# Kernel optimization log

Measured on AMD Instinct MI355X. Metric: run time of the kernel, lower is better.

## Reference

```python
import jax, jax.numpy as jnp
import numpy as np

B, H, W, C = 2, 64, 64, 256
G, K, L = 16, 9, 2
Cg = C // G


def _ln(x, g, b, eps=1e-6):
    m = jnp.mean(x, -1, keepdims=True)
    v = jnp.mean((x - m) ** 2, -1, keepdims=True)
    return (x - m) * jax.lax.rsqrt(v + eps) * g + b


def _conv(x, w, b=None, groups=1):
    y = jax.lax.conv_general_dilated(x, w, (1, 1), 'SAME',
        dimension_numbers=('NHWC', 'HWIO', 'NHWC'), feature_group_count=groups)
    return y if b is None else y + b


def _gelu(x):
    return jax.nn.gelu(x, approximate=False)  # torch nn.GELU (exact erf)


def _dcnv3(x, dw_w, dw_b, dwn_g, dwn_b, off_w, off_b, msk_w, msk_b,
           inp_w, inp_b, out_w, out_b, offset_scale=1.0):
    # x: [B,H,W,C] channels-last. kernel=3, stride=1, pad=1, dilation=1.
    xp = x @ inp_w + inp_b                                   # input_proj
    f = _gelu(_ln(_conv(x, dw_w, dw_b, groups=C), dwn_g, dwn_b))  # dw_conv branch
    off = (f @ off_w + off_b).reshape(B, H, W, G, K, 2) * offset_scale  # pixel units (x,y)
    mask = jax.nn.softmax((f @ msk_w + msk_b).reshape(B, H, W, G, K), axis=-1)
    dy, dx = jnp.meshgrid(jnp.arange(3.0) - 1.0, jnp.arange(3.0) - 1.0, indexing='ij')
    gx = dx.reshape(-1)
    gy = dy.reshape(-1)  # [K] kernel dilation grid
    # sampling locations in the zero-padded (pad=1) frame; pixel i center = i+0.5
    loc_x = (jnp.arange(W, dtype=x.dtype) + 1.5)[None, None, :, None, None] + gx + off[..., 0]
    loc_y = (jnp.arange(H, dtype=x.dtype) + 1.5)[None, :, None, None, None] + gy + off[..., 1]
    xg = jnp.pad(xp, ((0, 0), (1, 1), (1, 1), (0, 0))).reshape(B, H + 2, W + 2, G, Cg)
    px = loc_x - 0.5
    py = loc_y - 0.5
    x0 = jnp.floor(px).astype(jnp.int32)
    y0 = jnp.floor(py).astype(jnp.int32)
    fx = (px - x0)[..., None]
    fy = (py - y0)[..., None]
    Hp, Wp = H + 2, W + 2
    bi = jnp.arange(B).reshape(B, 1, 1, 1, 1)
    gi = jnp.arange(G).reshape(1, 1, 1, G, 1)

    def gather(yi, xi):  # zero padding outside bounds (grid_sample padding_mode='zeros')
        ok = ((yi >= 0) & (yi < Hp) & (xi >= 0) & (xi < Wp)).astype(x.dtype)[..., None]
        return xg[bi, jnp.clip(yi, 0, Hp - 1), jnp.clip(xi, 0, Wp - 1), gi] * ok

    top = gather(y0, x0) * (1 - fx) + gather(y0, x0 + 1) * fx
    bot = gather(y0 + 1, x0) * (1 - fx) + gather(y0 + 1, x0 + 1) * fx
    samp = top * (1 - fy) + bot * fy                         # [B,H,W,G,K,Cg]
    out = (samp * mask[..., None]).sum(4).reshape(B, H, W, C)
    return out @ out_w + out_b                               # output_proj


def _leffn(x, dc_w, dc_b, g, b, c1_w, c1_b, c2_w, c2_b, gamma):
    y = _ln(_conv(x, dc_w, dc_b, groups=C), g, b)
    y = _gelu(y @ c1_w + c1_b) @ c2_w + c2_b
    return x + gamma * y


def _cbam(x, w1, w2, sa_w, g, b):
    fc = lambda v: jax.nn.relu(v @ w1) @ w2
    ca = jax.nn.sigmoid(fc(x.mean((1, 2))) + fc(x.max((1, 2))))[:, None, None, :]
    x = x * ca
    sm = jnp.stack([x.mean(-1), x.max(-1)], -1)              # [B,H,W,2]
    x = x * jax.nn.sigmoid(_conv(sm, sa_w))
    return _ln(x, g, b)


def _upsample(x, w, bb, g, bt):
    y = jax.image.resize(x, (B, 2 * H, 2 * W, C), 'bilinear')  # align_corners=False
    y = _conv(y, w, bb)                                        # 3x3, C -> C//2
    return _gelu(_ln(y, g, bt))


def _forward(x, ln1_g, ln1_b, dw_w, dw_b, dwn_g, dwn_b, off_w, off_b, msk_w, msk_b,
             inp_w, inp_b, out_w, out_b, ln2_g, ln2_b, dc_w, dc_b, fn_g, fn_b,
             c1_w, c1_b, c2_w, c2_b, ffn_gamma, ca_w1, ca_w2, sa_w, cb_g, cb_b,
             nf_g, nf_b, up_w, up_b, up_g, up_bt):
    x = _cbam(x, ca_w1, ca_w2, sa_w, cb_g, cb_b)
    for i in range(L):  # fixed small depth; structural loop
        x = x + _dcnv3(_ln(x, ln1_g[i], ln1_b[i]), dw_w[i], dw_b[i], dwn_g[i], dwn_b[i],
                       off_w[i], off_b[i], msk_w[i], msk_b[i], inp_w[i], inp_b[i],
                       out_w[i], out_b[i])
        x = x + _leffn(_ln(x, ln2_g[i], ln2_b[i]), dc_w[i], dc_b[i], fn_g[i], fn_b[i],
                       c1_w[i], c1_b[i], c2_w[i], c2_b[i], ffn_gamma[i])
    x = _ln(x, nf_g, nf_b)
    return _upsample(x, up_w, up_b, up_g, up_bt)


def setup_inputs() -> dict:
    ks = iter(jax.random.split(jax.random.key(0), 80))
    r = lambda shp, s=0.02: jax.random.normal(next(ks), shp, dtype=jnp.float32) * s
    one = lambda shp: jnp.ones(shp, jnp.float32)
    zero = lambda shp: jnp.zeros(shp, jnp.float32)
    return dict(
        x=jax.random.normal(next(ks), (B, H, W, C), dtype=jnp.float32),
        ln1_g=one((L, C)), ln1_b=zero((L, C)),
        dw_w=r((L, 3, 3, 1, C)), dw_b=zero((L, C)),
        dwn_g=one((L, C)), dwn_b=zero((L, C)),
        off_w=r((L, C, G * K * 2), 0.01), off_b=zero((L, G * K * 2)),
        msk_w=r((L, C, G * K)), msk_b=zero((L, G * K)),
        inp_w=r((L, C, C)), inp_b=zero((L, C)),
        out_w=r((L, C, C)), out_b=zero((L, C)),
        ln2_g=one((L, C)), ln2_b=zero((L, C)),
        dc_w=r((L, 7, 7, 1, C)), dc_b=zero((L, C)),
        fn_g=one((L, C)), fn_b=zero((L, C)),
        c1_w=r((L, C, 4 * C)), c1_b=zero((L, 4 * C)),
        c2_w=r((L, 4 * C, C)), c2_b=zero((L, C)),
        ffn_gamma=0.7 * one((L, C)),
        ca_w1=r((C, C // 16)), ca_w2=r((C // 16, C)),
        sa_w=r((7, 7, 2, 1)),
        cb_g=one((C,)), cb_b=zero((C,)),
        nf_g=one((C,)), nf_b=zero((C,)),
        up_w=r((3, 3, C, C // 2)), up_b=zero((C // 2,)),
        up_g=one((C // 2,)), up_bt=zero((C // 2,)),
    )


def reference(x, ln1_g, ln1_b, dw_w, dw_b, dwn_g, dwn_b, off_w, off_b, msk_w, msk_b,
              inp_w, inp_b, out_w, out_b, ln2_g, ln2_b, dc_w, dc_b, fn_g, fn_b,
              c1_w, c1_b, c2_w, c2_b, ffn_gamma, ca_w1, ca_w2, sa_w, cb_g, cb_b,
              nf_g, nf_b, up_w, up_b, up_g, up_bt):
    return _forward(x, ln1_g, ln1_b, dw_w, dw_b, dwn_g, dwn_b, off_w, off_b, msk_w, msk_b,
                    inp_w, inp_b, out_w, out_b, ln2_g, ln2_b, dc_w, dc_b, fn_g, fn_b,
                    c1_w, c1_b, c2_w, c2_b, ffn_gamma, ca_w1, ca_w2, sa_w, cb_g, cb_b,
                    nf_g, nf_b, up_w, up_b, up_g, up_bt)
```

## Files before the change

### kernel.cpp

```cpp
#include <hip/hip_runtime.h>
#include <math.h>

#define B_ 2
#define H_ 64
#define W_ 64
#define C_ 256
#define G_ 16
#define HW_ (H_*W_)
#define M_ (B_*HW_)
#define C4_ (4*C_)
#define OFFN_ 288
#define MSKN_ 144
#define OMN_ 432
#define UH_ 128
#define UW_ 128
#define MUP_ (B_*UH_*UW_)
#define KUP_ (9*C_)
#define NOUT_ 128

typedef short short8 __attribute__((ext_vector_type(8)));
typedef float f32x4 __attribute__((ext_vector_type(4)));
typedef unsigned short us4 __attribute__((ext_vector_type(4)));

__device__ __forceinline__ float gelu_f(float x){
  return 0.5f * x * (1.f + erff(x * 0.70710678118654752440f));
}
__device__ __forceinline__ float sigmoid_f(float x){ return 1.f/(1.f+expf(-x)); }
__device__ __forceinline__ unsigned short f2bf(float x){
  unsigned int u = __float_as_uint(x);
  unsigned int r = (u + 0x7fffu + ((u>>16)&1u)) >> 16;
  return (unsigned short)r;
}
__device__ __forceinline__ float bf2f(unsigned short u){
  return __uint_as_float(((unsigned int)u) << 16);
}
__device__ __forceinline__ float bfl(unsigned int u){ return __uint_as_float(u<<16); }
__device__ __forceinline__ float bfh(unsigned int u){ return __uint_as_float(u & 0xffff0000u); }
__device__ __forceinline__ unsigned int pk(float a, float b){
  return (unsigned int)f2bf(a) | ((unsigned int)f2bf(b) << 16);
}

__device__ __forceinline__ void block_sum2(float& s, float& ss, float* sm){
  #pragma unroll
  for (int off=32; off>0; off>>=1){ s += __shfl_down(s, off); ss += __shfl_down(ss, off); }
  int lane = threadIdx.x & 63, wid = threadIdx.x >> 6;
  if (lane == 0){ sm[wid] = s; sm[4+wid] = ss; }
  __syncthreads();
  float a = 0.f, b = 0.f;
  int nw = blockDim.x >> 6;
  for (int i=0;i<nw;i++){ a += sm[i]; b += sm[4+i]; }
  s = a; ss = b;
}

__device__ __forceinline__ void block_summax(float& s, float& m, float* sm){
  #pragma unroll
  for (int off=32; off>0; off>>=1){ s += __shfl_down(s, off); m = fmaxf(m, __shfl_down(m, off)); }
  int lane = threadIdx.x & 63, wid = threadIdx.x >> 6;
  if (lane == 0){ sm[wid] = s; sm[4+wid] = m; }
  __syncthreads();
  float a = 0.f, b = -3.4e38f;
  int nw = blockDim.x >> 6;
  for (int i=0;i<nw;i++){ a += sm[i]; b = fmaxf(b, sm[4+i]); }
  s = a; m = b;
}

#define NJOBS 13
struct WtJobs {
  const float* src[NJOBS];
  unsigned short* dst[NJOBS];
  int Kd[NJOBS], Nd[NJOBS];
  int tOff[NJOBS+1];
};

__global__ __launch_bounds__(256) void k_wt_all(WtJobs J){
  __shared__ float tile[32][33];
  int bid = blockIdx.x;
  int j = 0;
  while (bid >= J.tOff[j+1]) j++;
  int lt = bid - J.tOff[j];
  const float* W = J.src[j];
  unsigned short* Wt = J.dst[j];
  int Kd = J.Kd[j], Nd = J.Nd[j];
  int ktiles = Kd >> 5;
  int k0 = (lt % ktiles) * 32, n0 = (lt / ktiles) * 32;
  int t = threadIdx.x;
  int r = t>>3, c4 = (t&7)*4;
  float4 v = make_float4(0.f,0.f,0.f,0.f);
  if (n0 + c4 < Nd) v = *(const float4*)(W + (size_t)(k0+r)*Nd + n0 + c4);
  tile[c4+0][r]=v.x; tile[c4+1][r]=v.y; tile[c4+2][r]=v.z; tile[c4+3][r]=v.w;
  __syncthreads();
  if (n0 + r < Nd){
    us4 o;
    o.x = f2bf(tile[r][c4+0]); o.y = f2bf(tile[r][c4+1]);
    o.z = f2bf(tile[r][c4+2]); o.w = f2bf(tile[r][c4+3]);
    *(us4*)(Wt + (size_t)(n0+r)*Kd + k0 + c4) = o;
  }
}

__global__ __launch_bounds__(256) void k_chpool(const float* __restrict__ Xin,
      float* __restrict__ psum, float* __restrict__ pmax){
  int chunk = blockIdx.x, b = blockIdx.y; int c = threadIdx.x;
  const float* p = Xin + (((size_t)b*HW_) + chunk*32)*C_ + c;
  float s = 0.f, m = -3.4e38f;
  for (int i=0;i<32;i++){ float v = p[(size_t)i*C_]; s += v; m = fmaxf(m, v); }
  psum[(b*128+chunk)*C_+c] = s; pmax[(b*128+chunk)*C_+c] = m;
}

__global__ __launch_bounds__(512) void k_ca(const float* __restrict__ psum, const float* __restrict__ pmax,
    const float* __restrict__ w1, const float* __restrict__ w2, float* __restrict__ ca){
  __shared__ float pm[2][256], px[2][256], hh[2][2][16];
  int t = threadIdx.x;
  {
    int b = t >> 8, c = t & 255;
    float s = 0.f, m = -3.4e38f;
    for (int ch=0; ch<128; ch++){ s += psum[(b*128+ch)*256+c]; m = fmaxf(m, pmax[(b*128+ch)*256+c]); }
    pm[b][c] = s * (1.f/4096.f); px[b][c] = m;
  }
  __syncthreads();
  if (t < 64){
    int b = t >> 5, typ = (t >> 4) & 1, j = t & 15;
    const float* src = typ ? px[b] : pm[b];
    float a = 0.f;
    for (int c2=0;c2<256;c2++) a += src[c2]*w1[c2*16+j];
    hh[b][typ][j] = fmaxf(a, 0.f);
  }
  __syncthreads();
  {
    int b = t >> 8, c = t & 255;
    float a = 0.f;
    for (int j=0;j<16;j++) a += (hh[b][0][j]+hh[b][1][j]) * w2[j*256+c];
    ca[b*256+c] = sigmoid_f(a);
  }
}

__global__ __launch_bounds__(256) void k_apply_ca(const float* __restrict__ Xin, float* __restrict__ X,
    const float* __restrict__ ca, float* __restrict__ smean, float* __restrict__ smax){
  __shared__ float sm[12];
  int pix = blockIdx.x, c = threadIdx.x;
  int b = pix >> 12;
  float v = Xin[(size_t)pix*C_+c] * ca[b*C_+c];
  X[(size_t)pix*C_+c] = v;
  float s = v, m = v;
  block_summax(s, m, sm);
  if (c == 0){ smean[pix] = s * (1.f/C_); smax[pix] = m; }
}

__global__ __launch_bounds__(256) void k_sa(const float* __restrict__ smean, const float* __restrict__ smax,
    const float* __restrict__ w, float* __restrict__ sa){
  int pix = blockIdx.x*256 + threadIdx.x;
  if (pix >= M_) return;
  int b = pix >> 12, hw = pix & 4095, h = hw >> 6, ww = hw & 63;
  float s = 0.f;
  for (int ky=0;ky<7;ky++){
    int hh = h + ky - 3; if (hh < 0 || hh >= H_) continue;
    for (int kx=0;kx<7;kx++){
      int xx = ww + kx - 3; if (xx < 0 || xx >= W_) continue;
      int q = (b<<12) + (hh<<6) + xx;
      s += smean[q]*w[(ky*7+kx)*2+0] + smax[q]*w[(ky*7+kx)*2+1];
    }
  }
  sa[pix] = sigmoid_f(s);
}

__global__ __launch_bounds__(256) void k_mul_ln_ln1(float* __restrict__ X, const float* __restrict__ sa,
    const float* __restrict__ g, const float* __restrict__ b,
    const float* __restrict__ g1, const float* __restrict__ b1, unsigned short* __restrict__ Tb){
  __shared__ float sm[12];
  int pix = blockIdx.x, c = threadIdx.x;
  float v = X[(size_t)pix*C_+c] * sa[pix];
  float s = v, ss = v*v;
  block_sum2(s, ss, sm);
  float mean = s * (1.f/C_), var = ss*(1.f/C_) - mean*mean;
  float r = rsqrtf(var + 1e-6f);
  float x0 = (v-mean)*r*g[c] + b[c];
  X[(size_t)pix*C_+c] = x0;
  __syncthreads();
  s = x0; ss = x0*x0;
  block_sum2(s, ss, sm);
  mean = s * (1.f/C_); var = ss*(1.f/C_) - mean*mean;
  r = rsqrtf(var + 1e-6f);
  Tb[(size_t)pix*C_+c] = f2bf((x0-mean)*r*g1[c] + b1[c]);
}

template<int KS, int DOGELU>
__global__ __launch_bounds__(256) void k_dwconv(const unsigned short* __restrict__ T,
    unsigned short* __restrict__ Out,
    const float* __restrict__ w, const float* __restrict__ bias,
    const float* __restrict__ g, const float* __restrict__ bb){
  constexpr int R = KS/2;
  int t = blockIdx.x*256 + threadIdx.x;
  int pix = t >> 5, grp = t & 31;
  int c0 = grp*8;
  int b = pix >> 12, hw = pix & 4095, h = hw >> 6, ww = hw & 63;
  float acc[8];
  {
    float4 b0 = *(const float4*)(bias + c0), b1 = *(const float4*)(bias + c0 + 4);
    acc[0]=b0.x; acc[1]=b0.y; acc[2]=b0.z; acc[3]=b0.w;
    acc[4]=b1.x; acc[5]=b1.y; acc[6]=b1.z; acc[7]=b1.w;
  }
  const unsigned short* tb = T + ((size_t)b*HW_)*C_ + c0;
  for (int ky=0;ky<KS;ky++){
    int hh = h + ky - R; if (hh < 0 || hh >= H_) continue;
    for (int kx=0;kx<KS;kx++){
      int xx = ww + kx - R; if (xx < 0 || xx >= W_) continue;
      uint4 a = *(const uint4*)(tb + ((size_t)hh*W_+xx)*C_);
      const float* wp = w + (ky*KS+kx)*C_ + c0;
      float4 w0 = *(const float4*)wp, w1 = *(const float4*)(wp+4);
      acc[0] += bfl(a.x)*w0.x; acc[1] += bfh(a.x)*w0.y;
      acc[2] += bfl(a.y)*w0.z; acc[3] += bfh(a.y)*w0.w;
      acc[4] += bfl(a.z)*w1.x; acc[5] += bfh(a.z)*w1.y;
      acc[6] += bfl(a.w)*w1.z; acc[7] += bfh(a.w)*w1.w;
    }
  }
  float s = 0.f, ss = 0.f;
  #pragma unroll
  for (int i=0;i<8;i++){ s += acc[i]; ss += acc[i]*acc[i]; }
  #pragma unroll
  for (int off=1; off<32; off<<=1){ s += __shfl_xor(s, off); ss += __shfl_xor(ss, off); }
  float mean = s * (1.f/C_), var = ss*(1.f/C_) - mean*mean;
  float r = rsqrtf(var + 1e-6f);
  float4 g0 = *(const float4*)(g + c0), g1 = *(const float4*)(g + c0 + 4);
  float4 p0 = *(const float4*)(bb + c0), p1 = *(const float4*)(bb + c0 + 4);
  float o[8];
  o[0]=(acc[0]-mean)*r*g0.x+p0.x; o[1]=(acc[1]-mean)*r*g0.y+p0.y;
  o[2]=(acc[2]-mean)*r*g0.z+p0.z; o[3]=(acc[3]-mean)*r*g0.w+p0.w;
  o[4]=(acc[4]-mean)*r*g1.x+p1.x; o[5]=(acc[5]-mean)*r*g1.y+p1.y;
  o[6]=(acc[6]-mean)*r*g1.z+p1.z; o[7]=(acc[7]-mean)*r*g1.w+p1.w;
  if (DOGELU){
    #pragma unroll
    for (int i=0;i<8;i++) o[i] = gelu_f(o[i]);
  }
  uint4 ov;
  ov.x = pk(o[0],o[1]); ov.y = pk(o[2],o[3]); ov.z = pk(o[4],o[5]); ov.w = pk(o[6],o[7]);
  *(uint4*)(Out + (size_t)pix*C_ + c0) = ov;
}

template<int TM, int EP, int OUTBF>
__global__ __launch_bounds__(256) void k_gemm_mfma(
    const unsigned short* __restrict__ A, const unsigned short* __restrict__ Bt,
    void* __restrict__ OutV, const float* __restrict__ bias,
    const float* __restrict__ bias2, int Ni, int Ki)
{
  constexpr int LD = 40;
  __shared__ unsigned short As[TM*LD];
  __shared__ unsigned short Bs[128*LD];
  const int tid = threadIdx.x;
  const int wave = tid >> 6, lane = tid & 63;
  const int m0 = blockIdx.x * TM, n0 = blockIdx.y * 128;
  const int wm0 = (wave >> 1) * (TM/2);
  const int wn0 = (wave & 1) * 64;
  constexpr int MI = TM/32;
  f32x4 acc[MI][4] = {};
  const int lm = lane & 15, kq = lane >> 4;
  constexpr int ACH = TM*4/256;

  for (int k0 = 0; k0 < Ki; k0 += 32){
    #pragma unroll
    for (int i=0;i<ACH;i++){
      int ch = tid*ACH + i;
      int r = ch >> 2, cc = (ch & 3) << 3;
      short8 v = *(const short8*)(A + (size_t)(m0 + r)*Ki + k0 + cc);
      *(short8*)(As + r*LD + cc) = v;
    }
    #pragma unroll
    for (int i=0;i<2;i++){
      int ch = tid + 256*i;
      int r = ch >> 2, cc = (ch & 3) << 3;
      short8 v = {};
      if (n0 + r < Ni) v = *(const short8*)(Bt + (size_t)(n0 + r)*Ki + k0 + cc);
      *(short8*)(Bs + r*LD + cc) = v;
    }
    __syncthreads();
    short8 af[MI], bf[4];
    #pragma unroll
    for (int mi=0;mi<MI;mi++) af[mi] = *(const short8*)(As + (wm0 + mi*16 + lm)*LD + kq*8);
    #pragma unroll
    for (int ni=0;ni<4;ni++)  bf[ni] = *(const short8*)(Bs + (wn0 + ni*16 + lm)*LD + kq*8);
    #pragma unroll
    for (int mi=0;mi<MI;mi++)
      #pragma unroll
      for (int ni=0;ni<4;ni++)
        acc[mi][ni] = __builtin_amdgcn_mfma_f32_16x16x32_bf16(af[mi], bf[ni], acc[mi][ni], 0,0,0);
    __syncthreads();
  }
  #pragma unroll
  for (int mi=0;mi<MI;mi++){
    #pragma unroll
    for (int ni=0;ni<4;ni++){
      int n = n0 + wn0 + ni*16 + lm;
      if (n < Ni){
        float bv;
        if constexpr (EP==4) bv = (n < OFFN_) ? bias[n] : bias2[n-OFFN_];
        else bv = bias[n];
        #pragma unroll
        for (int r=0;r<4;r++){
          int m = m0 + wm0 + mi*16 + kq*4 + r;
          size_t o = (size_t)m*Ni + n;
          float v = acc[mi][ni][r] + bv;
          if constexpr (EP==1) v = gelu_f(v);
          if constexpr (OUTBF) ((unsigned short*)OutV)[o] = f2bf(v);
          else                 ((float*)OutV)[o] = v;
        }
      }
    }
  }
}

template<int EP>
__global__ __launch_bounds__(256) void k_gemm_ln(
    const unsigned short* __restrict__ A, const unsigned short* __restrict__ Bt,
    float* __restrict__ X, const float* __restrict__ bias,
    const unsigned short* __restrict__ res2b, const float* __restrict__ gamma,
    unsigned short* __restrict__ OutTb,
    const float* __restrict__ lng, const float* __restrict__ lnb, int Ki)
{
  constexpr int LD = 40;
  __shared__ unsigned short As[32*LD];
  __shared__ unsigned short Bs[256*LD];
  __shared__ float rs[32][2], rq[32][2];
  const int tid = threadIdx.x;
  const int wave = tid >> 6, lane = tid & 63;
  const int m0 = blockIdx.x * 32;
  const int wm0 = (wave >> 1) * 16;
  const int wn0 = (wave & 1) * 128;
  const int lm = lane & 15, kq = lane >> 4;
  f32x4 acc[8] = {};

  for (int k0 = 0; k0 < Ki; k0 += 32){
    if (tid < 128){
      int r = tid >> 2, cc = (tid & 3) << 3;
      short8 v = *(const short8*)(A + (size_t)(m0 + r)*Ki + k0 + cc);
      *(short8*)(As + r*LD + cc) = v;
    }
    #pragma unroll
    for (int i=0;i<4;i++){
      int ch = tid + 256*i;
      int r = ch >> 2, cc = (ch & 3) << 3;
      short8 v = *(const short8*)(Bt + (size_t)r*Ki + k0 + cc);
      *(short8*)(Bs + r*LD + cc) = v;
    }
    __syncthreads();
    short8 af = *(const short8*)(As + (wm0 + lm)*LD + kq*8);
    short8 bf[8];
    #pragma unroll
    for (int ni=0;ni<8;ni++) bf[ni] = *(const short8*)(Bs + (wn0 + ni*16 + lm)*LD + kq*8);
    #pragma unroll
    for (int ni=0;ni<8;ni++)
      acc[ni] = __builtin_amdgcn_mfma_f32_16x16x32_bf16(af, bf[ni], acc[ni], 0,0,0);
    __syncthreads();
  }
  int nn[8]; float bv[8], gv[8];
  #pragma unroll
  for (int ni=0;ni<8;ni++){
    nn[ni] = wn0 + ni*16 + lm;
    bv[ni] = bias[nn[ni]];
    if constexpr (EP==3) gv[ni] = gamma[nn[ni]];
  }
  float ps[4] = {}, pq[4] = {};
  #pragma unroll
  for (int r=0;r<4;r++){
    int m = m0 + wm0 + kq*4 + r;
    #pragma unroll
    for (int ni=0;ni<8;ni++){
      size_t o = (size_t)m*C_ + nn[ni];
      float v = acc[ni][r] + bv[ni];
      if constexpr (EP==2) v = X[o] + v;
      if constexpr (EP==3) v = X[o] + bf2f(res2b[o]) + gv[ni]*v;
      X[o] = v;
      acc[ni][r] = v;
      ps[r] += v; pq[r] += v*v;
    }
  }
  #pragma unroll
  for (int off=1; off<16; off<<=1){
    #pragma unroll
    for (int r=0;r<4;r++){ ps[r] += __shfl_xor(ps[r], off); pq[r] += __shfl_xor(pq[r], off); }
  }
  if (lm == 0){
    #pragma unroll
    for (int r=0;r<4;r++){
      rs[wm0 + kq*4 + r][wave & 1] = ps[r];
      rq[wm0 + kq*4 + r][wave & 1] = pq[r];
    }
  }
  __syncthreads();
  float lg[8], lb[8];
  #pragma unroll
  for (int ni=0;ni<8;ni++){ lg[ni] = lng[nn[ni]]; lb[ni] = lnb[nn[ni]]; }
  #pragma unroll
  for (int r=0;r<4;r++){
    int row = wm0 + kq*4 + r;
    int m = m0 + row;
    float s = rs[row][0] + rs[row][1];
    float q = rq[row][0] + rq[row][1];
    float mean = s * (1.f/C_), var = q*(1.f/C_) - mean*mean;
    float rstd = rsqrtf(var + 1e-6f);
    #pragma unroll
    for (int ni=0;ni<8;ni++){
      size_t o = (size_t)m*C_ + nn[ni];
      OutTb[o] = f2bf((acc[ni][r]-mean)*rstd*lg[ni] + lb[ni]);
    }
  }
}

__global__ __launch_bounds__(256) void k_dcn(const unsigned short* __restrict__ xp,
    const float* __restrict__ OM, unsigned short* __restrict__ S){
  __shared__ float lom[16*OMN_];
  int pix0 = blockIdx.x * 16;
  {
    const float* gsrc = OM + (size_t)pix0*OMN_;
    for (int idx = threadIdx.x; idx < 16*OMN_; idx += 256) lom[idx] = gsrc[idx];
  }
  __syncthreads();
  int pl = threadIdx.x >> 4, g = threadIdx.x & 15;
  int pix = pix0 + pl;
  int b = pix >> 12, hw = pix & 4095, h = hw >> 6, ww = hw & 63;
  const float* offp = lom + pl*OMN_ + g*18;
  const float* mp   = lom + pl*OMN_ + OFFN_ + g*9;
  const unsigned short* xpb = xp + ((size_t)b*HW_)*C_ + g*16;
  float e[9]; float mx = -3.4e38f;
  #pragma unroll
  for (int k=0;k<9;k++){ e[k] = mp[k]; mx = fmaxf(mx, e[k]); }
  float ssum = 0.f;
  #pragma unroll
  for (int k=0;k<9;k++){ e[k] = expf(e[k]-mx); ssum += e[k]; }
  float rinv = 1.f/ssum;
  float acc[16] = {};
  #pragma unroll
  for (int k=0;k<9;k++){
    float ox = offp[k*2+0], oy = offp[k*2+1];
    float px = (float)(ww + (k%3)) + ox;
    float py = (float)(h  + (k/3)) + oy;
    int x0 = (int)floorf(px), y0 = (int)floorf(py);
    float fx = px - (float)x0, fy = py - (float)y0;
    float mk = e[k]*rinv;
    float w00 = mk*(1.f-fx)*(1.f-fy), w01 = mk*fx*(1.f-fy);
    float w10 = mk*(1.f-fx)*fy,       w11 = mk*fx*fy;
    #define CORNER(yy,xx,WGT) do{ \
      if ((yy)>=1 && (yy)<=H_ && (xx)>=1 && (xx)<=W_){ \
        const unsigned short* p = xpb + ((size_t)((yy)-1)*W_ + ((xx)-1))*C_; \
        uint4 a0 = *(const uint4*)p; uint4 a1 = *(const uint4*)(p+8); \
        acc[0]+=WGT*bfl(a0.x); acc[1]+=WGT*bfh(a0.x); acc[2]+=WGT*bfl(a0.y); acc[3]+=WGT*bfh(a0.y); \
        acc[4]+=WGT*bfl(a0.z); acc[5]+=WGT*bfh(a0.z); acc[6]+=WGT*bfl(a0.w); acc[7]+=WGT*bfh(a0.w); \
        acc[8]+=WGT*bfl(a1.x); acc[9]+=WGT*bfh(a1.x); acc[10]+=WGT*bfl(a1.y); acc[11]+=WGT*bfh(a1.y); \
        acc[12]+=WGT*bfl(a1.z); acc[13]+=WGT*bfh(a1.z); acc[14]+=WGT*bfl(a1.w); acc[15]+=WGT*bfh(a1.w); \
      } \
    }while(0)
    CORNER(y0,   x0,   w00);
    CORNER(y0,   x0+1, w01);
    CORNER(y0+1, x0,   w10);
    CORNER(y0+1, x0+1, w11);
    #undef CORNER
  }
  unsigned short* sp = S + (size_t)pix*C_ + g*16;
  uint4 o0, o1;
  o0.x = pk(acc[0],acc[1]);   o0.y = pk(acc[2],acc[3]);
  o0.z = pk(acc[4],acc[5]);   o0.w = pk(acc[6],acc[7]);
  o1.x = pk(acc[8],acc[9]);   o1.y = pk(acc[10],acc[11]);
  o1.z = pk(acc[12],acc[13]); o1.w = pk(acc[14],acc[15]);
  *(uint4*)sp = o0;
  *(uint4*)(sp+8) = o1;
}

__global__ __launch_bounds__(256) void k_upsample(const unsigned short* __restrict__ T, unsigned short* __restrict__ U){
  int t = blockIdx.x*256 + threadIdx.x;
  int opix = t >> 5, grp = t & 31;
  int c0 = grp*8;
  int ox = opix & 127, oy = (opix >> 7) & 127, b = opix >> 14;
  float sy = oy*0.5f - 0.25f, sx = ox*0.5f - 0.25f;
  int y0 = (int)floorf(sy), x0 = (int)floorf(sx);
  float fy = sy - (float)y0, fx = sx - (float)x0;
  int y0c = min(max(y0,0),H_-1), y1c = min(max(y0+1,0),H_-1);
  int x0c = min(max(x0,0),W_-1), x1c = min(max(x0+1,0),W_-1);
  const unsigned short* tb = T + ((size_t)b*HW_)*C_ + c0;
  uint4 q00 = *(const uint4*)(tb + ((size_t)y0c*W_+x0c)*C_);
  uint4 q01 = *(const uint4*)(tb + ((size_t)y0c*W_+x1c)*C_);
  uint4 q10 = *(const uint4*)(tb + ((size_t)y1c*W_+x0c)*C_);
  uint4 q11 = *(const uint4*)(tb + ((size_t)y1c*W_+x1c)*C_);
  float w00=(1.f-fy)*(1.f-fx), w01=(1.f-fy)*fx, w10=fy*(1.f-fx), w11=fy*fx;
  float o[8];
  o[0]=w00*bfl(q00.x)+w01*bfl(q01.x)+w10*bfl(q10.x)+w11*bfl(q11.x);
  o[1]=w00*bfh(q00.x)+w01*bfh(q01.x)+w10*bfh(q10.x)+w11*bfh(q11.x);
  o[2]=w00*bfl(q00.y)+w01*bfl(q01.y)+w10*bfl(q10.y)+w11*bfl(q11.y);
  o[3]=w00*bfh(q00.y)+w01*bfh(q01.y)+w10*bfh(q10.y)+w11*bfh(q11.y);
  o[4]=w00*bfl(q00.z)+w01*bfl(q01.z)+w10*bfl(q10.z)+w11*bfl(q11.z);
  o[5]=w00*bfh(q00.z)+w01*bfh(q01.z)+w10*bfh(q10.z)+w11*bfh(q11.z);
  o[6]=w00*bfl(q00.w)+w01*bfl(q01.w)+w10*bfl(q10.w)+w11*bfl(q11.w);
  o[7]=w00*bfh(q00.w)+w01*bfh(q01.w)+w10*bfh(q10.w)+w11*bfh(q11.w);
  uint4 ov;
  ov.x = pk(o[0],o[1]); ov.y = pk(o[2],o[3]); ov.z = pk(o[4],o[5]); ov.w = pk(o[6],o[7]);
  *(uint4*)(U + (size_t)opix*C_ + c0) = ov;
}

__global__ __launch_bounds__(256) void k_upconv_ln(
    const unsigned short* __restrict__ U, const unsigned short* __restrict__ Wt,
    float* __restrict__ Out, const float* __restrict__ bias,
    const float* __restrict__ g, const float* __restrict__ bb)
{
  constexpr int LD = 72;
  __shared__ unsigned short As[64*LD];
  __shared__ unsigned short Bs[128*LD];
  __shared__ float rs[64][2], rq[64][2];
  const int tid = threadIdx.x;
  const int wave = tid >> 6, lane = tid & 63;
  const int m0 = blockIdx.x * 64;
  const int wm0 = (wave >> 1) * 32;
  const int wn0 = (wave & 1) * 64;
  const int lm = lane & 15, kq = lane >> 4;
  f32x4 acc[2][4] = {};
  const int r0 = tid >> 3, cA = (tid & 7) << 3;
  int bar[2], oyr[2], oxr[2];
  #pragma unroll
  for (int i=0;i<2;i++){
    int m = m0 + r0 + 32*i;
    bar[i] = m >> 14; oyr[i] = (m >> 7) & 127; oxr[i] = m & 127;
  }

  for (int k0 = 0; k0 < KUP_; k0 += 64){
    int tap = k0 >> 8, cc0 = k0 & 255;
    int dy = tap/3 - 1, dx = tap%3 - 1;
    #pragma unroll
    for (int i=0;i<2;i++){
      int iy = oyr[i] + dy, ix = oxr[i] + dx;
      short8 v = {};
      if (iy >= 0 && iy < UH_ && ix >= 0 && ix < UW_)
        v = *(const short8*)(U + (((size_t)bar[i]*UH_ + iy)*UW_ + ix)*C_ + cc0 + cA);
      *(short8*)(As + (r0 + 32*i)*LD + cA) = v;
    }
    #pragma unroll
    for (int i=0;i<4;i++){
      int r = r0 + 32*i;
      short8 v = *(const short8*)(Wt + (size_t)r*KUP_ + k0 + cA);
      *(short8*)(Bs + r*LD + cA) = v;
    }
    __syncthreads();
    short8 af[2][2], bf[4][2];
    #pragma unroll
    for (int mi=0;mi<2;mi++)
      #pragma unroll
      for (int kk=0;kk<2;kk++)
        af[mi][kk] = *(const short8*)(As + (wm0 + mi*16 + lm)*LD + kk*32 + kq*8);
    #pragma unroll
    for (int ni=0;ni<4;ni++)
      #pragma unroll
      for (int kk=0;kk<2;kk++)
        bf[ni][kk] = *(const short8*)(Bs + (wn0 + ni*16 + lm)*LD + kk*32 + kq*8);
    #pragma unroll
    for (int kk=0;kk<2;kk++)
      #pragma unroll
      for (int mi=0;mi<2;mi++)
        #pragma unroll
        for (int ni=0;ni<4;ni++)
          acc[mi][ni] = __builtin_amdgcn_mfma_f32_16x16x32_bf16(af[mi][kk], bf[ni][kk], acc[mi][ni], 0,0,0);
    __syncthreads();
  }
  int nn[4]; float bv[4];
  #pragma unroll
  for (int ni=0;ni<4;ni++){ nn[ni] = wn0 + ni*16 + lm; bv[ni] = bias[nn[ni]]; }
  float ps[2][4] = {}, pq[2][4] = {};
  #pragma unroll
  for (int mi=0;mi<2;mi++)
    #pragma unroll
    for (int r=0;r<4;r++)
      #pragma unroll
      for (int ni=0;ni<4;ni++){
        float v = acc[mi][ni][r] + bv[ni];
        acc[mi][ni][r] = v;
        ps[mi][r] += v; pq[mi][r] += v*v;
      }
  #pragma unroll
  for (int off=1; off<16; off<<=1){
    #pragma unroll
    for (int mi=0;mi<2;mi++)
      #pragma unroll
      for (int r=0;r<4;r++){ ps[mi][r] += __shfl_xor(ps[mi][r], off); pq[mi][r] += __shfl_xor(pq[mi][r], off); }
  }
  if (lm == 0){
    #pragma unroll
    for (int mi=0;mi<2;mi++)
      #pragma unroll
      for (int r=0;r<4;r++){
        rs[wm0 + mi*16 + kq*4 + r][wave & 1] = ps[mi][r];
        rq[wm0 + mi*16 + kq*4 + r][wave & 1] = pq[mi][r];
      }
  }
  __syncthreads();
  float gv[4], pv[4];
  #pragma unroll
  for (int ni=0;ni<4;ni++){ gv[ni] = g[nn[ni]]; pv[ni] = bb[nn[ni]]; }
  #pragma unroll
  for (int mi=0;mi<2;mi++)
    #pragma unroll
    for (int r=0;r<4;r++){
      int row = wm0 + mi*16 + kq*4 + r;
      int m = m0 + row;
      float s = rs[row][0] + rs[row][1];
      float q = rq[row][0] + rq[row][1];
      float mean = s * (1.f/NOUT_), var = q*(1.f/NOUT_) - mean*mean;
      float rstd = rsqrtf(var + 1e-6f);
      #pragma unroll
      for (int ni=0;ni<4;ni++)
        Out[(size_t)m*NOUT_ + nn[ni]] = gelu_f((acc[mi][ni][r]-mean)*rstd*gv[ni] + pv[ni]);
    }
}

extern "C" void kernel_launch(void* const* d_in, const int* in_sizes, int n_in,
                              void* d_out, int out_size, void* d_ws, size_t ws_size,
                              hipStream_t stream)
{
  (void)in_sizes; (void)n_in; (void)out_size; (void)ws_size;
  const float* x_in = (const float*)d_in[0];
  char* w = (char*)d_ws;
  const size_t MB = 1u<<20;
  float* X    = (float*)(w + 0*MB);
  float* OM   = (float*)(w + 8*MB);
  unsigned short* MIDb = (unsigned short*)(w + 22*MB);
  unsigned short* Ub   = MIDb;
  unsigned short* Tb   = (unsigned short*)(w + 38*MB);
  unsigned short* Fb   = (unsigned short*)(w + 42*MB);
  unsigned short* XPb  = (unsigned short*)(w + 46*MB);
  unsigned short* DW7b = (unsigned short*)(w + 50*MB);
  unsigned short* Sb   = (unsigned short*)(w + 54*MB);
  unsigned short* WT   = (unsigned short*)(w + 58*MB);
  float* psum = (float*)(w + 62*MB);
  float* pmax = psum + 65536;
  float* ca   = pmax + 65536;
  float* smean= ca + 512;
  float* smax = smean + 8192;
  float* sa   = smax + 8192;

  unsigned short* WtInp[2], *WtOut[2], *WtOM[2], *WtC1[2], *WtC2[2];
  {
    size_t o = 0;
    for (int i=0;i<2;i++){
      WtInp[i] = WT + o; o += 65536;
      WtOut[i] = WT + o; o += 65536;
      WtOM[i]  = WT + o; o += 110592;
      WtC1[i]  = WT + o; o += 262144;
      WtC2[i]  = WT + o; o += 262144;
    }
  }
  unsigned short* WtUp = WT + 1531904;

  WtJobs J;
  {
    int ji = 0, toff = 0;
    auto add = [&](const float* s, unsigned short* d, int Kd, int Nd){
      J.src[ji]=s; J.dst[ji]=d; J.Kd[ji]=Kd; J.Nd[ji]=Nd;
      J.tOff[ji]=toff; toff += (Kd>>5) * ((Nd+31)>>5); ji++;
    };
    for (int i=0;i<2;i++){
      add((const float*)d_in[11] + (size_t)i*C_*C_,   WtInp[i], C_, C_);
      add((const float*)d_in[13] + (size_t)i*C_*C_,   WtOut[i], C_, C_);
      add((const float*)d_in[7]  + (size_t)i*C_*OFFN_, WtOM[i], C_, OFFN_);
      add((const float*)d_in[9]  + (size_t)i*C_*MSKN_, WtOM[i] + (size_t)OFFN_*C_, C_, MSKN_);
      add((const float*)d_in[21] + (size_t)i*C_*C4_,  WtC1[i], C_, C4_);
      add((const float*)d_in[23] + (size_t)i*C4_*C_,  WtC2[i], C4_, C_);
    }
    add((const float*)d_in[33], WtUp, KUP_, NOUT_);
    J.tOff[ji] = toff;
    k_wt_all<<<toff,256,0,stream>>>(J);
  }

  k_chpool<<<dim3(128,2),256,0,stream>>>(x_in, psum, pmax);
  k_ca<<<1,512,0,stream>>>(psum, pmax, (const float*)d_in[26], (const float*)d_in[27], ca);
  k_apply_ca<<<M_,256,0,stream>>>(x_in, X, ca, smean, smax);
  k_sa<<<M_/256,256,0,stream>>>(smean, smax, (const float*)d_in[28], sa);
  k_mul_ln_ln1<<<M_,256,0,stream>>>(X, sa, (const float*)d_in[29], (const float*)d_in[30],
      (const float*)d_in[1], (const float*)d_in[2], Tb);

  for (int i=0;i<2;i++){
    const float* dww  = (const float*)d_in[3] + i*9*C_;
    const float* dwb  = (const float*)d_in[4] + i*C_;
    const float* dwng = (const float*)d_in[5] + i*C_;
    const float* dwnb = (const float*)d_in[6] + i*C_;
    const float* offb = (const float*)d_in[8] + i*OFFN_;
    const float* mskb = (const float*)d_in[10] + i*MSKN_;
    const float* inpb = (const float*)d_in[12] + i*C_;
    const float* outb = (const float*)d_in[14] + i*C_;
    const float* ln2g = (const float*)d_in[15] + i*C_;
    const float* ln2b = (const float*)d_in[16] + i*C_;
    const float* dcw  = (const float*)d_in[17] + i*49*C_;
    const float* dcb  = (const float*)d_in[18] + i*C_;
    const float* fng  = (const float*)d_in[19] + i*C_;
    const float* fnb  = (const float*)d_in[20] + i*C_;
    const float* c1b  = (const float*)d_in[22] + i*C4_;
    const float* c2b  = (const float*)d_in[24] + i*C_;
    const float* gam  = (const float*)d_in[25] + i*C_;
    const float* nxg = (i==0) ? (const float*)d_in[1] + C_ : (const float*)d_in[31];
    const float* nxb = (i==0) ? (const float*)d_in[2] + C_ : (const float*)d_in[32];

    k_gemm_mfma<64,0,1><<<dim3(M_/64,2),256,0,stream>>>(Tb, WtInp[i], XPb, inpb, nullptr, C_, C_);
    k_dwconv<3,1><<<M_*32/256,256,0,stream>>>(Tb, Fb, dww, dwb, dwng, dwnb);
    k_gemm_mfma<64,4,0><<<dim3(M_/64,4),256,0,stream>>>(Fb, WtOM[i], OM, offb, mskb, OMN_, C_);
    k_dcn<<<M_/16,256,0,stream>>>(XPb, OM, Sb);
    k_gemm_ln<2><<<M_/32,256,0,stream>>>(Sb, WtOut[i], X, outb, nullptr, nullptr, Tb, ln2g, ln2b, C_);

    k_dwconv<7,0><<<M_*32/256,256,0,stream>>>(Tb, DW7b, dcw, dcb, fng, fnb);
    k_gemm_mfma<128,1,1><<<dim3(M_/128,8),256,0,stream>>>(DW7b, WtC1[i], MIDb, c1b, nullptr, C4_, C_);
    k_gemm_ln<3><<<M_/32,256,0,stream>>>(MIDb, WtC2[i], X, c2b, Tb, gam, Tb, nxg, nxb, C4_);
  }

  k_upsample<<<MUP_*32/256,256,0,stream>>>(Tb, Ub);
  k_upconv_ln<<<MUP_/64,256,0,stream>>>(Ub, WtUp, (float*)d_out, (const float*)d_in[34],
      (const float*)d_in[35], (const float*)d_in[36]);
}
```

Baseline: 520.5 us.

## Widen K-step and use 8 waves in GEMM+LN; double K-tile in upconv

The fused GEMM+LayerNorm kernel moves to 512 threads with a 4-way N split across waves and a K-step of 64 instead of 32, so there are half as many barrier/load iterations and more waves per block. The row statistics reduction is widened to 4 partials to match. The upconv kernel's K-tile doubles to 128 per iteration with 32-channel contiguous A loads per thread. The generic GEMM's A-load loop is generalized. LDS use grows, which may lower occupancy.

```diff
diff --git a/kernel.cpp b/kernel.cpp
--- a/kernel.cpp
+++ b/kernel.cpp
@@ -249,15 +249,12 @@
   const int m0 = blockIdx.x * TM, n0 = blockIdx.y * 128;
   const int wm0 = (wave >> 1) * (TM/2);
   const int wn0 = (wave & 1) * 64;
-  constexpr int MI = TM/32;
+  constexpr int MI = (TM+31)/32;
   f32x4 acc[MI][4] = {};
   const int lm = lane & 15, kq = lane >> 4;
-  constexpr int ACH = TM*4/256;
 
   for (int k0 = 0; k0 < Ki; k0 += 32){
-    #pragma unroll
-    for (int i=0;i<ACH;i++){
-      int ch = tid*ACH + i;
+    for (int ch = tid; ch < TM*4; ch += 256){
       int r = ch >> 2, cc = (ch & 3) << 3;
       short8 v = *(const short8*)(A + (size_t)(m0 + r)*Ki + k0 + cc);
       *(short8*)(As + r*LD + cc) = v;
@@ -307,51 +304,58 @@
 }
 
 template<int EP>
-__global__ __launch_bounds__(256) void k_gemm_ln(
+__global__ __launch_bounds__(512) void k_gemm_ln(
     const unsigned short* __restrict__ A, const unsigned short* __restrict__ Bt,
     float* __restrict__ X, const float* __restrict__ bias,
     const unsigned short* __restrict__ res2b, const float* __restrict__ gamma,
     unsigned short* __restrict__ OutTb,
     const float* __restrict__ lng, const float* __restrict__ lnb, int Ki)
 {
-  constexpr int LD = 40;
+  constexpr int LD = 72;
   __shared__ unsigned short As[32*LD];
   __shared__ unsigned short Bs[256*LD];
-  __shared__ float rs[32][2], rq[32][2];
+  __shared__ float rs[32][4], rq[32][4];
   const int tid = threadIdx.x;
   const int wave = tid >> 6, lane = tid & 63;
   const int m0 = blockIdx.x * 32;
-  const int wm0 = (wave >> 1) * 16;
-  const int wn0 = (wave & 1) * 128;
+  const int wm0 = (wave >> 2) * 16;
+  const int wn0 = (wave & 3) * 64;
   const int lm = lane & 15, kq = lane >> 4;
-  f32x4 acc[8] = {};
-
-  for (int k0 = 0; k0 < Ki; k0 += 32){
-    if (tid < 128){
-      int r = tid >> 2, cc = (tid & 3) << 3;
+  f32x4 acc[4] = {};
+
+  for (int k0 = 0; k0 < Ki; k0 += 64){
+    if (tid < 256){
+      int r = tid >> 3, cc = (tid & 7) << 3;
       short8 v = *(const short8*)(A + (size_t)(m0 + r)*Ki + k0 + cc);
       *(short8*)(As + r*LD + cc) = v;
     }
     #pragma unroll
     for (int i=0;i<4;i++){
-      int ch = tid + 256*i;
-      int r = ch >> 2, cc = (ch & 3) << 3;
+      int ch = tid + 512*i;
+      int r = ch >> 3, cc = (ch & 7) << 3;
       short8 v = *(const short8*)(Bt + (size_t)r*Ki + k0 + cc);
       *(short8*)(Bs + r*LD + cc) = v;
     }
     __syncthreads();
-    short8 af = *(const short8*)(As + (wm0 + lm)*LD + kq*8);
-    short8 bf[8];
-    #pragma unroll
-    for (int ni=0;ni<8;ni++) bf[ni] = *(const short8*)(Bs + (wn0 + ni*16 + lm)*LD + kq*8);
-    #pragma unroll
-    for (int ni=0;ni<8;ni++)
-      acc[ni] = __builtin_amdgcn_mfma_f32_16x16x32_bf16(af, bf[ni], acc[ni], 0,0,0);
+    short8 af[2], bf4[4][2];
+    #pragma unroll
+    for (int kk=0;kk<2;kk++)
+      af[kk] = *(const short8*)(As + (wm0 + lm)*LD + kk*32 + kq*8);
+    #pragma unroll
+    for (int ni=0;ni<4;ni++)
+      #pragma unroll
+      for (int kk=0;kk<2;kk++)
+        bf4[ni][kk] = *(const short8*)(Bs + (wn0 + ni*16 + lm)*LD + kk*32 + kq*8);
+    #pragma unroll
+    for (int kk=0;kk<2;kk++)
+      #pragma unroll
+      for (int ni=0;ni<4;ni++)
+        acc[ni] = __builtin_amdgcn_mfma_f32_16x16x32_bf16(af[kk], bf4[ni][kk], acc[ni], 0,0,0);
     __syncthreads();
   }
-  int nn[8]; float bv[8], gv[8];
-  #pragma unroll
-  for (int ni=0;ni<8;ni++){
+  int nn[4]; float bv[4], gv[4];
+  #pragma unroll
+  for (int ni=0;ni<4;ni++){
     nn[ni] = wn0 + ni*16 + lm;
     bv[ni] = bias[nn[ni]];
     if constexpr (EP==3) gv[ni] = gamma[nn[ni]];
@@ -361,7 +365,7 @@
   for (int r=0;r<4;r++){
     int m = m0 + wm0 + kq*4 + r;
     #pragma unroll
-    for (int ni=0;ni<8;ni++){
+    for (int ni=0;ni<4;ni++){
       size_t o = (size_t)m*C_ + nn[ni];
       float v = acc[ni][r] + bv[ni];
       if constexpr (EP==2) v = X[o] + v;
@@ -379,24 +383,24 @@
   if (lm == 0){
     #pragma unroll
     for (int r=0;r<4;r++){
-      rs[wm0 + kq*4 + r][wave & 1] = ps[r];
-      rq[wm0 + kq*4 + r][wave & 1] = pq[r];
-    }
-  }
-  __syncthreads();
-  float lg[8], lb[8];
-  #pragma unroll
-  for (int ni=0;ni<8;ni++){ lg[ni] = lng[nn[ni]]; lb[ni] = lnb[nn[ni]]; }
+      rs[wm0 + kq*4 + r][wave & 3] = ps[r];
+      rq[wm0 + kq*4 + r][wave & 3] = pq[r];
+    }
+  }
+  __syncthreads();
+  float lg[4], lb[4];
+  #pragma unroll
+  for (int ni=0;ni<4;ni++){ lg[ni] = lng[nn[ni]]; lb[ni] = lnb[nn[ni]]; }
   #pragma unroll
   for (int r=0;r<4;r++){
     int row = wm0 + kq*4 + r;
     int m = m0 + row;
-    float s = rs[row][0] + rs[row][1];
-    float q = rq[row][0] + rq[row][1];
+    float s = rs[row][0] + rs[row][1] + rs[row][2] + rs[row][3];
+    float q = rq[row][0] + rq[row][1] + rq[row][2] + rq[row][3];
     float mean = s * (1.f/C_), var = q*(1.f/C_) - mean*mean;
     float rstd = rsqrtf(var + 1e-6f);
     #pragma unroll
-    for (int ni=0;ni<8;ni++){
+    for (int ni=0;ni<4;ni++){
       size_t o = (size_t)m*C_ + nn[ni];
       OutTb[o] = f2bf((acc[ni][r]-mean)*rstd*lg[ni] + lb[ni]);
     }
@@ -497,7 +501,7 @@
     float* __restrict__ Out, const float* __restrict__ bias,
     const float* __restrict__ g, const float* __restrict__ bb)
 {
-  constexpr int LD = 72;
+  constexpr int LD = 136;
   __shared__ unsigned short As[64*LD];
   __shared__ unsigned short Bs[128*LD];
   __shared__ float rs[64][2], rq[64][2];
@@ -508,50 +512,50 @@
   const int wn0 = (wave & 1) * 64;
   const int lm = lane & 15, kq = lane >> 4;
   f32x4 acc[2][4] = {};
-  const int r0 = tid >> 3, cA = (tid & 7) << 3;
-  int bar[2], oyr[2], oxr[2];
-  #pragma unroll
-  for (int i=0;i<2;i++){
-    int m = m0 + r0 + 32*i;
-    bar[i] = m >> 14; oyr[i] = (m >> 7) & 127; oxr[i] = m & 127;
-  }
-
-  for (int k0 = 0; k0 < KUP_; k0 += 64){
+  const int r0 = tid >> 2, cA0 = (tid & 3) << 5;
+  const int ma = m0 + r0;
+  const int ba = ma >> 14, oya = (ma >> 7) & 127, oxa = ma & 127;
+
+  for (int k0 = 0; k0 < KUP_; k0 += 128){
     int tap = k0 >> 8, cc0 = k0 & 255;
     int dy = tap/3 - 1, dx = tap%3 - 1;
-    #pragma unroll
-    for (int i=0;i<2;i++){
-      int iy = oyr[i] + dy, ix = oxr[i] + dx;
-      short8 v = {};
-      if (iy >= 0 && iy < UH_ && ix >= 0 && ix < UW_)
-        v = *(const short8*)(U + (((size_t)bar[i]*UH_ + iy)*UW_ + ix)*C_ + cc0 + cA);
-      *(short8*)(As + (r0 + 32*i)*LD + cA) = v;
-    }
-    #pragma unroll
-    for (int i=0;i<4;i++){
-      int r = r0 + 32*i;
-      short8 v = *(const short8*)(Wt + (size_t)r*KUP_ + k0 + cA);
-      *(short8*)(Bs + r*LD + cA) = v;
+    {
+      int iy = oya + dy, ix = oxa + dx;
+      bool ok = (iy >= 0 && iy < UH_ && ix >= 0 && ix < UW_);
+      const unsigned short* src = U + (((size_t)ba*UH_ + iy)*UW_ + ix)*C_ + cc0 + cA0;
+      #pragma unroll
+      for (int i=0;i<4;i++){
+        short8 v = {};
+        if (ok) v = *(const short8*)(src + i*8);
+        *(short8*)(As + r0*LD + cA0 + i*8) = v;
+      }
+    }
+    #pragma unroll
+    for (int i=0;i<8;i++){
+      int ch = tid + 256*i;
+      int r = ch >> 4, cc = (ch & 15) << 3;
+      short8 v = *(const short8*)(Wt + (size_t)r*KUP_ + k0 + cc);
+      *(short8*)(Bs + r*LD + cc) = v;
     }
     __syncthreads();
-    short8 af[2][2], bf[4][2];
+    short8 af[2][4], bf4[4][4];
     #pragma unroll
     for (int mi=0;mi<2;mi++)
       #pragma unroll
-      for (int kk=0;kk<2;kk++)
+      for (int kk=0;kk<4;kk++)
         af[mi][kk] = *(const short8*)(As + (wm0 + mi*16 + lm)*LD + kk*32 + kq*8);
     #pragma unroll
     for (int ni=0;ni<4;ni++)
       #pragma unroll
-      for (int kk=0;kk<2;kk++)
-        bf[ni][kk] = *(const short8*)(Bs + (wn0 + ni*16 + lm)*LD + kk*32 + kq*8);
-    #pragma unroll
-    for (int kk=0;kk<2;kk++)
+      for (int kk=0;kk<4;kk++)
+        bf4[ni][kk] = *(const short8*)(Bs + (wn0 + ni*16 + lm)*LD + kk*32 + kq*8);
+    #pragma unroll
+    for (int kk=0;kk<4;kk++)
       #pragma unroll
       for (int mi=0;mi<2;mi++)
         #pragma unroll
         for (int ni=0;ni<4;ni++)
-          acc[mi][ni] = __builtin_amdgcn_mfma_f32_16x16x32_bf16(af[mi][kk], bf[ni][kk], acc[mi][ni], 0,0,0);
+          acc[mi][ni] = __builtin_amdgcn_mfma_f32_16x16x32_bf16(af[mi][kk], bf4[ni][kk], acc[mi][ni], 0,0,0);
     __syncthreads();
   }
   int nn[4]; float bv[4];
@@ -694,11 +698,11 @@
     k_dwconv<3,1><<<M_*32/256,256,0,stream>>>(Tb, Fb, dww, dwb, dwng, dwnb);
     k_gemm_mfma<64,4,0><<<dim3(M_/64,4),256,0,stream>>>(Fb, WtOM[i], OM, offb, mskb, OMN_, C_);
     k_dcn<<<M_/16,256,0,stream>>>(XPb, OM, Sb);
-    k_gemm_ln<2><<<M_/32,256,0,stream>>>(Sb, WtOut[i], X, outb, nullptr, nullptr, Tb, ln2g, ln2b, C_);
+    k_gemm_ln<2><<<M_/32,512,0,stream>>>(Sb, WtOut[i], X, outb, nullptr, nullptr, Tb, ln2g, ln2b, C_);
 
     k_dwconv<7,0><<<M_*32/256,256,0,stream>>>(Tb, DW7b, dcw, dcb, fng, fnb);
     k_gemm_mfma<128,1,1><<<dim3(M_/128,8),256,0,stream>>>(DW7b, WtC1[i], MIDb, c1b, nullptr, C4_, C_);
-    k_gemm_ln<3><<<M_/32,256,0,stream>>>(MIDb, WtC2[i], X, c2b, Tb, gam, Tb, nxg, nxb, C4_);
+    k_gemm_ln<3><<<M_/32,512,0,stream>>>(MIDb, WtC2[i], X, c2b, Tb, gam, Tb, nxg, nxb, C4_);
   }
 
   k_upsample<<<MUP_*32/256,256,0,stream>>>(Tb, Ub);
```

Measured after the change: 568.4 us. 9.2% more time.
